# Kernel optimization log

Hardware: AMD Instinct MI355X
Metric: run time of the kernel (lower is better)

## Reference

```python
import jax, jax.numpy as jnp
import numpy as np

N, E, IN = 50000, 800000, 64
HC, FC1, FC2, FC3, OUT = 96, 256, 128, 64, 8
EPS = 1e-5


def setup_inputs() -> dict:
    key = jax.random.key(0)
    ks = jax.random.split(key, 24)
    def lin(k, fi, fo):
        # kaiming_uniform with relu gain: bound = sqrt(6/fi)
        b = np.sqrt(6.0 / fi)
        return jax.random.uniform(k, (fi, fo), jnp.float32, -b, b)
    inp = {
        'x': jax.random.normal(ks[0], (N, IN), jnp.float32),
        'edge_index': jax.random.randint(ks[1], (2, E), 0, N, jnp.int64),
        'w1': lin(ks[2], IN, HC), 'b1': jnp.zeros((HC,), jnp.float32),
        'g1': jax.random.uniform(ks[3], (HC,), jnp.float32, 0.5, 1.5), 'be1': jax.random.normal(ks[4], (HC,), jnp.float32) * 0.1,
        'w2': lin(ks[5], HC, HC), 'b2': jnp.zeros((HC,), jnp.float32),
        'g2': jax.random.uniform(ks[6], (HC,), jnp.float32, 0.5, 1.5), 'be2': jax.random.normal(ks[7], (HC,), jnp.float32) * 0.1,
        'w3': lin(ks[8], HC, HC), 'b3': jnp.zeros((HC,), jnp.float32),
        'g3': jax.random.uniform(ks[9], (HC,), jnp.float32, 0.5, 1.5), 'be3': jax.random.normal(ks[10], (HC,), jnp.float32) * 0.1,
        'lw1': lin(ks[11], HC, FC1), 'lb1': jnp.zeros((FC1,), jnp.float32),
        'lw2': lin(ks[12], FC1, FC2), 'lb2': jnp.zeros((FC2,), jnp.float32),
        'lw3': lin(ks[13], FC2, FC3), 'lb3': jnp.zeros((FC3,), jnp.float32),
        'lw4': lin(ks[14], FC3, OUT), 'lb4': jnp.zeros((OUT,), jnp.float32),
    }
    return inp


def _gcn(x, w, b, src, dst, norm):
    # GCNConv: out[dst] += norm_e * (x @ w)[src]; then + bias
    h = x @ w
    msg = h[src] * norm[:, None]
    return jax.ops.segment_sum(msg, dst, num_segments=N) + b


def _bn_eval(x, g, be):
    # eval-mode BatchNorm1d with running_mean=0, running_var=1
    return x / jnp.sqrt(1.0 + EPS) * g + be


def reference(x, edge_index, w1, b1, g1, be1, w2, b2, g2, be2, w3, b3, g3, be3,
              lw1, lb1, lw2, lb2, lw3, lb3, lw4, lb4):
    loops = jnp.arange(N, dtype=edge_index.dtype)
    src = jnp.concatenate([edge_index[0], loops])
    dst = jnp.concatenate([edge_index[1], loops])
    deg = jax.ops.segment_sum(jnp.ones_like(src, jnp.float32), dst, num_segments=N)
    dinv = jax.lax.rsqrt(deg)  # deg >= 1 due to self loops
    norm = dinv[src] * dinv[dst]

    h = jax.nn.relu(_bn_eval(_gcn(x, w1, b1, src, dst, norm), g1, be1))
    h = jax.nn.relu(_bn_eval(_gcn(h, w2, b2, src, dst, norm), g2, be2))
    h = jax.nn.relu(_bn_eval(_gcn(h, w3, b3, src, dst, norm), g3, be3))
    h = jax.nn.relu(h @ lw1 + lb1)
    h = jax.nn.relu(h @ lw2 + lb2)
    h = jax.nn.relu(h @ lw3 + lb3)
    return h @ lw4 + lb4
```

## Files before the change

kernel.cpp:

```cpp
#include <hip/hip_runtime.h>


#define GN 50000
#define GE 800000
#define NPART 98
#define PSLOT 9216
#define CHK 2048

typedef __attribute__((ext_vector_type(8))) short bf16x8;
typedef __attribute__((ext_vector_type(4))) float floatx4;

__device__ __forceinline__ float ar1_b2f(unsigned short h) {
    return __uint_as_float(((unsigned)h) << 16);
}
__device__ __forceinline__ unsigned short ar1_f2b(float f) {
    unsigned u = __float_as_uint(f);
    u = u + 0x7FFFu + ((u >> 16) & 1u);
    return (unsigned short)(u >> 16);
}

__device__ __forceinline__ int ar1_det64(const int* ei) {
    int l = (int)threadIdx.x & 63;
    int nz = 0;
#pragma unroll
    for (int k = 0; k < 4; k++)
        nz += (ei[2 * (l + 64 * k) + 1] != 0) ? 1 : 0;
#pragma unroll
    for (int o = 1; o < 64; o <<= 1)
        nz += __shfl_xor(nz, o, 64);
    return (nz < 8) ? 1 : 0;
}
__device__ __forceinline__ int ar1_detf32(const unsigned short* xw) {
    int l = (int)threadIdx.x & 63;
    int c = 0;
#pragma unroll
    for (int k = 0; k < 4; k++) {
        unsigned short w = xw[2 * (l + 64 * k)];
        int ex = (w >> 7) & 0xFF;
        if (w == 0 || (ex >= 90 && ex <= 150)) c++;
    }
#pragma unroll
    for (int o = 1; o < 64; o <<= 1)
        c += __shfl_xor(c, o, 64);
    return (c > 200) ? 0 : 1;
}

struct PackAll {
    const void* src[7];
    unsigned short* dst[7];
    int K[7], M[7], start[8];
};
struct SmallCvt {
    const void* src[4];
    float* dst[4];
    int n[4];
    const void* gb[9];
    float* ss[6];
};

__global__ __launch_bounds__(256)
void Arthur1_16458314678864_kernel(PackAll pa, SmallCvt sc,
                                   const int* __restrict__ ei,
                                   const unsigned short* __restrict__ xw,
                                   int* flagI, int* flagF,
                                   int* __restrict__ gcur,
                                   unsigned int* __restrict__ pairs,
                                   unsigned short* __restrict__ xb) {
    int b = (int)blockIdx.x;
    int tid = (int)threadIdx.x;
    if (b < 391) {
        __shared__ int cnt[NPART], base[NPART], cur[NPART];
        for (int i = tid; i < NPART; i += 256) { cnt[i] = 0; cur[i] = 0; }
        int is64 = ar1_det64(ei);
        __syncthreads();
        int e0 = b * CHK;
        unsigned pk[8]; int q[8];
#pragma unroll
        for (int k = 0; k < 8; k++) {
            int e = e0 + k * 256 + tid;
            q[k] = -1; pk[k] = 0;
            if (e < GE) {
                int s = is64 ? ei[2 * e] : ei[e];
                int d = is64 ? ei[2 * (GE + e)] : ei[GE + e];
                if ((unsigned)s < (unsigned)GN && (unsigned)d < (unsigned)GN) {
                    int qq = d >> 9;
                    q[k] = qq;
                    pk[k] = (unsigned)s | ((unsigned)(d & 511) << 17);
                    atomicAdd(&cnt[qq], 1);
                }
            }
        }
        __syncthreads();
        for (int i = tid; i < NPART; i += 256)
            base[i] = (cnt[i] > 0) ? atomicAdd(&gcur[i], cnt[i]) : 0;
        __syncthreads();
#pragma unroll
        for (int k = 0; k < 8; k++) {
            if (q[k] >= 0) {
                int r = base[q[k]] + atomicAdd(&cur[q[k]], 1);
                if (r < PSLOT) pairs[(size_t)q[k] * PSLOT + r] = pk[k];
            }
        }
    } else if (b < 436) {
        int f = ar1_detf32(xw);
        int frag_g = (b - 391) * 4 + (tid >> 6);
        if (frag_g >= 178) return;
        int w = 0;
        while (w < 6 && frag_g >= pa.start[w + 1]) w++;
        int frag = frag_g - pa.start[w];
        int K = pa.K[w], M = pa.M[w];
        int lane = tid & 63;
        int nch = K >> 5;
        int t = frag / nch, c = frag - t * nch;
        int n = t * 16 + (lane & 15);
        int k0 = c * 32 + (lane >> 4) * 8;
        unsigned short* o = pa.dst[w] + ((size_t)frag * 64 + lane) * 8;
        for (int j = 0; j < 8; j++) {
            unsigned short v = 0;
            if (n < M) {
                int idx = (k0 + j) * M + n;
                v = f ? ar1_f2b(((const float*)pa.src[w])[idx])
                      : ((const unsigned short*)pa.src[w])[idx];
            }
            o[j] = v;
        }
    } else if (b == 436) {
        int f = ar1_detf32(xw);
        int i64 = ar1_det64(ei);
        if (tid == 0) { flagI[0] = i64; flagF[0] = f; }
        const float C = 0.9999950000374997f;
        for (int s = 0; s < 4; s++) {
            for (int i = tid; i < sc.n[s]; i += 256) {
                float v = f ? ((const float*)sc.src[s])[i]
                            : ar1_b2f(((const unsigned short*)sc.src[s])[i]);
                sc.dst[s][i] = v;
            }
        }
        for (int k = 0; k < 3; k++) {
            for (int i = tid; i < 96; i += 256) {
                float bb, g, be;
                if (f) {
                    bb = ((const float*)sc.gb[3 * k + 0])[i];
                    g  = ((const float*)sc.gb[3 * k + 1])[i];
                    be = ((const float*)sc.gb[3 * k + 2])[i];
                } else {
                    bb = ar1_b2f(((const unsigned short*)sc.gb[3 * k + 0])[i]);
                    g  = ar1_b2f(((const unsigned short*)sc.gb[3 * k + 1])[i]);
                    be = ar1_b2f(((const unsigned short*)sc.gb[3 * k + 2])[i]);
                }
                sc.ss[2 * k + 0][i] = C * g;
                sc.ss[2 * k + 1][i] = bb * C * g + be;
            }
        }
    } else {
        int f = ar1_detf32(xw);
        size_t t = (size_t)(b - 437) * 256 + (size_t)tid;
        size_t i0 = t * 8;
        if (i0 < (size_t)GN * 64) {
            bf16x8 o;
            if (f) {
                const float* xf = (const float*)xw;
                floatx4 a = *((const floatx4*)(xf + i0));
                floatx4 c = *((const floatx4*)(xf + i0 + 4));
#pragma unroll
                for (int j = 0; j < 4; j++) {
                    o[j]     = (short)ar1_f2b(a[j]);
                    o[4 + j] = (short)ar1_f2b(c[j]);
                }
            } else {
                o = *((const bf16x8*)(xw + i0));
            }
            *((bf16x8*)(xb + i0)) = o;
        }
    }
}

__global__ __launch_bounds__(256)
void ar1_csr(const unsigned int* __restrict__ pairs, const int* __restrict__ gcur,
             int* __restrict__ csr, int* __restrict__ indeg,
             int* __restrict__ offs, float* __restrict__ dinv) {
    __shared__ int ncnt[512], pre[512], cur[512], psum[16], red[256];
    int p = (int)blockIdx.x, tid = (int)threadIdx.x;
    red[tid] = (tid < p && tid < NPART) ? gcur[tid] : 0;
    __syncthreads();
    for (int o = 128; o > 0; o >>= 1) {
        if (tid < o) red[tid] += red[tid + o];
        __syncthreads();
    }
    int gbase = red[0];
    int cntE = gcur[p];
    if (cntE > PSLOT) cntE = PSLOT;
    for (int i = tid; i < 512; i += 256) ncnt[i] = 0;
    __syncthreads();
    const unsigned int* pp = pairs + (size_t)p * PSLOT;
    for (int i = tid; i < cntE; i += 256) atomicAdd(&ncnt[pp[i] >> 17], 1);
    __syncthreads();
    if (tid < 16) {
        int s = 0;
        for (int j = tid * 32; j < tid * 32 + 32; j++) { pre[j] = s; s += ncnt[j]; }
        psum[tid] = s;
    }
    __syncthreads();
    if (tid == 0) {
        int s = 0;
        for (int j = 0; j < 16; j++) { int t = psum[j]; psum[j] = s; s += t; }
    }
    __syncthreads();
    if (tid < 16)
        for (int j = tid * 32; j < tid * 32 + 32; j++) pre[j] += psum[tid];
    __syncthreads();
    for (int j = tid; j < 512; j += 256) {
        cur[j] = pre[j];
        int node = p * 512 + j;
        if (node < GN) {
            indeg[node] = ncnt[j];
            offs[node] = gbase + pre[j];
            dinv[node] = rsqrtf((float)(ncnt[j] + 1));
        }
    }
    __syncthreads();
    for (int i = tid; i < cntE; i += 256) {
        unsigned v = pp[i];
        int r = atomicAdd(&cur[v >> 17], 1);
        csr[gbase + r] = (int)(v & 0x1FFFFu);
    }
}

__global__ __launch_bounds__(1024, 8)
void ar1_ag64g(const unsigned short* __restrict__ Xb, const int* __restrict__ offs,
               const int* __restrict__ indeg, const int* __restrict__ csr,
               const float* __restrict__ dinv,
               const unsigned short* __restrict__ Bp,
               const float* __restrict__ scale, const float* __restrict__ shift,
               unsigned short* __restrict__ C) {
    __shared__ unsigned short AL[16 * 72];
    int tid = (int)threadIdx.x, wv = tid >> 6, lane = tid & 63;
    int nb = (int)blockIdx.x * 16;
    int node = nb + wv;
    int chunk = lane & 7, eslot = lane >> 3;
    float di = dinv[node];
    int off = offs[node], cnt = indeg[node];

    float acc[8];
#pragma unroll
    for (int j = 0; j < 8; j++) acc[j] = 0.f;

    for (int base = 0; base < cnt; base += 16) {
        int ss[2]; float ww[2];
#pragma unroll
        for (int k = 0; k < 2; k++) {
            int e = base + k * 8 + eslot;
            int s = node; float w = 0.f;
            if (e < cnt) {
                s = csr[off + e];
                if ((unsigned)s >= (unsigned)GN) s = node;
                w = dinv[s] * di;
            }
            ss[k] = s; ww[k] = w;
        }
#pragma unroll
        for (int k = 0; k < 2; k++) {
            bf16x8 h = *((const bf16x8*)(Xb + (size_t)ss[k] * 64 + chunk * 8));
#pragma unroll
            for (int j = 0; j < 8; j++)
                acc[j] += ww[k] * ar1_b2f((unsigned short)h[j]);
        }
    }
#pragma unroll
    for (int j = 0; j < 8; j++) {
        acc[j] += __shfl_xor(acc[j], 8, 64);
        acc[j] += __shfl_xor(acc[j], 16, 64);
        acc[j] += __shfl_xor(acc[j], 32, 64);
    }
    if (eslot == 0) {
        bf16x8 h = *((const bf16x8*)(Xb + (size_t)node * 64 + chunk * 8));
        bf16x8 o;
#pragma unroll
        for (int j = 0; j < 8; j++)
            o[j] = (short)ar1_f2b(acc[j] + di * di * ar1_b2f((unsigned short)h[j]));
        *((bf16x8*)(AL + (size_t)wv * 72 + chunk * 8)) = o;
    }
    __syncthreads();

    if (wv < 6) {
        int m = lane & 15, quad = lane >> 4, t = wv;
        floatx4 g = (floatx4){0.f, 0.f, 0.f, 0.f};
#pragma unroll
        for (int c = 0; c < 2; c++) {
            bf16x8 a = *((const bf16x8*)(AL + (size_t)m * 72 + c * 32 + quad * 8));
            bf16x8 bfr = *((const bf16x8*)(Bp + ((size_t)(t * 2 + c) * 64 + lane) * 8));
            g = __builtin_amdgcn_mfma_f32_16x16x32_bf16(a, bfr, g, 0, 0, 0);
        }
#pragma unroll
        for (int r = 0; r < 4; r++) {
            int row = nb + quad * 4 + r;
            int col = t * 16 + m;
            float v = g[r] * scale[col] + shift[col];
            C[(size_t)row * 96 + col] = ar1_f2b(fmaxf(v, 0.f));
        }
    }
}

__global__ __launch_bounds__(1024, 8)
void ar1_ag96g(const unsigned short* __restrict__ H, const int* __restrict__ offs,
               const int* __restrict__ indeg, const int* __restrict__ csr,
               const float* __restrict__ dinv,
               const unsigned short* __restrict__ Bp,
               const float* __restrict__ scale, const float* __restrict__ shift,
               unsigned short* __restrict__ C) {
    __shared__ unsigned short AL[16 * 104];
    int tid = (int)threadIdx.x, wv = tid >> 6, lane = tid & 63;
    int nb = (int)blockIdx.x * 16;
    int node = nb + wv;
    int chunk = lane % 12, eslot = lane / 12;
    int active = (lane < 48) ? 1 : 0;
    float di = dinv[node];
    int off = offs[node], cnt = indeg[node];

    float acc[8];
#pragma unroll
    for (int j = 0; j < 8; j++) acc[j] = 0.f;

    if (active) {
        for (int base = 0; base < cnt; base += 16) {
            int ss[4]; float ww[4]; bf16x8 hh[4];
#pragma unroll
            for (int k = 0; k < 4; k++) {
                int e = base + k * 4 + eslot;
                int s = node; float w = 0.f;
                if (e < cnt) {
                    s = csr[off + e];
                    if ((unsigned)s >= (unsigned)GN) s = node;
                    w = dinv[s] * di;
                }
                ss[k] = s; ww[k] = w;
            }
#pragma unroll
            for (int k = 0; k < 4; k++)
                hh[k] = *((const bf16x8*)(H + (size_t)ss[k] * 96 + chunk * 8));
#pragma unroll
            for (int k = 0; k < 4; k++)
#pragma unroll
                for (int j = 0; j < 8; j++)
                    acc[j] += ww[k] * ar1_b2f((unsigned short)hh[k][j]);
        }
    }
#pragma unroll
    for (int j = 0; j < 8; j++) {
        float a1 = __shfl(acc[j], lane + 12, 64);
        float a2 = __shfl(acc[j], lane + 24, 64);
        float a3 = __shfl(acc[j], lane + 36, 64);
        acc[j] += a1 + a2 + a3;
    }
    if (lane < 12) {
        bf16x8 hs = *((const bf16x8*)(H + (size_t)node * 96 + chunk * 8));
        bf16x8 o;
#pragma unroll
        for (int j = 0; j < 8; j++)
            o[j] = (short)ar1_f2b(acc[j] + di * di * ar1_b2f((unsigned short)hs[j]));
        *((bf16x8*)(AL + (size_t)wv * 104 + chunk * 8)) = o;
    }
    __syncthreads();

    if (wv < 6) {
        int m = lane & 15, quad = lane >> 4, t = wv;
        floatx4 g = (floatx4){0.f, 0.f, 0.f, 0.f};
#pragma unroll
        for (int c = 0; c < 3; c++) {
            bf16x8 a = *((const bf16x8*)(AL + (size_t)m * 104 + c * 32 + quad * 8));
            bf16x8 bfr = *((const bf16x8*)(Bp + ((size_t)(t * 3 + c) * 64 + lane) * 8));
            g = __builtin_amdgcn_mfma_f32_16x16x32_bf16(a, bfr, g, 0, 0, 0);
        }
#pragma unroll
        for (int r = 0; r < 4; r++) {
            int row = nb + quad * 4 + r;
            int col = t * 16 + m;
            float v = g[r] * scale[col] + shift[col];
            C[(size_t)row * 96 + col] = ar1_f2b(fmaxf(v, 0.f));
        }
    }
}

__global__ __launch_bounds__(1024, 8)
void ar1_agmlp(const unsigned short* __restrict__ H, const int* __restrict__ offs,
               const int* __restrict__ indeg, const int* __restrict__ csr,
               const float* __restrict__ dinv,
               const unsigned short* __restrict__ b2w,
               const float* __restrict__ sc3, const float* __restrict__ sh3,
               const unsigned short* __restrict__ b3,
               const unsigned short* __restrict__ b4,
               const unsigned short* __restrict__ b5,
               const unsigned short* __restrict__ b6,
               const float* __restrict__ lb0, const float* __restrict__ lb1,
               const float* __restrict__ lb2, const float* __restrict__ lb3,
               void* __restrict__ out, const int* __restrict__ f32out) {
    __shared__ unsigned short AL[16 * 104];
    __shared__ unsigned short H0[16 * 104];
    __shared__ unsigned short H1[16 * 264];
    __shared__ unsigned short H2[16 * 136];
    __shared__ unsigned short H3[16 * 72];
    int tid = (int)threadIdx.x, wv = tid >> 6, lane = tid & 63;
    int nb = (int)blockIdx.x * 16;
    int node = nb + wv;
    int m = lane & 15, quad = lane >> 4;

    {
        int chunk = lane % 12, eslot = lane / 12;
        int active = (lane < 48) ? 1 : 0;
        float di = dinv[node];
        int off = offs[node], cnt = indeg[node];
        float acc[8];
#pragma unroll
        for (int j = 0; j < 8; j++) acc[j] = 0.f;
        if (active) {
            for (int base = 0; base < cnt; base += 16) {
                int ss[4]; float ww[4]; bf16x8 hh[4];
#pragma unroll
                for (int k = 0; k < 4; k++) {
                    int e = base + k * 4 + eslot;
                    int s = node; float w = 0.f;
                    if (e < cnt) {
                        s = csr[off + e];
                        if ((unsigned)s >= (unsigned)GN) s = node;
                        w = dinv[s] * di;
                    }
                    ss[k] = s; ww[k] = w;
                }
#pragma unroll
                for (int k = 0; k < 4; k++)
                    hh[k] = *((const bf16x8*)(H + (size_t)ss[k] * 96 + chunk * 8));
#pragma unroll
                for (int k = 0; k < 4; k++)
#pragma unroll
                    for (int j = 0; j < 8; j++)
                        acc[j] += ww[k] * ar1_b2f((unsigned short)hh[k][j]);
            }
        }
#pragma unroll
        for (int j = 0; j < 8; j++) {
            float a1 = __shfl(acc[j], lane + 12, 64);
            float a2 = __shfl(acc[j], lane + 24, 64);
            float a3 = __shfl(acc[j], lane + 36, 64);
            acc[j] += a1 + a2 + a3;
        }
        if (lane < 12) {
            bf16x8 hs = *((const bf16x8*)(H + (size_t)node * 96 + chunk * 8));
            bf16x8 o;
#pragma unroll
            for (int j = 0; j < 8; j++)
                o[j] = (short)ar1_f2b(acc[j] + di * di * ar1_b2f((unsigned short)hs[j]));
            *((bf16x8*)(AL + (size_t)wv * 104 + chunk * 8)) = o;
        }
    }
    __syncthreads();

    if (wv < 6) {
        int t = wv;
        floatx4 g = (floatx4){0.f, 0.f, 0.f, 0.f};
#pragma unroll
        for (int c = 0; c < 3; c++) {
            bf16x8 a = *((const bf16x8*)(AL + (size_t)m * 104 + c * 32 + quad * 8));
            bf16x8 bfr = *((const bf16x8*)(b2w + ((size_t)(t * 3 + c) * 64 + lane) * 8));
            g = __builtin_amdgcn_mfma_f32_16x16x32_bf16(a, bfr, g, 0, 0, 0);
        }
#pragma unroll
        for (int r = 0; r < 4; r++) {
            int col = t * 16 + m;
            float v = g[r] * sc3[col] + sh3[col];
            H0[(quad * 4 + r) * 104 + col] = ar1_f2b(fmaxf(v, 0.f));
        }
    }
    __syncthreads();

    {
        int t = wv;
        floatx4 g = (floatx4){0.f, 0.f, 0.f, 0.f};
#pragma unroll
        for (int c = 0; c < 3; c++) {
            bf16x8 a = *((const bf16x8*)(H0 + (size_t)m * 104 + c * 32 + quad * 8));
            bf16x8 bfr = *((const bf16x8*)(b3 + ((size_t)(t * 3 + c) * 64 + lane) * 8));
            g = __builtin_amdgcn_mfma_f32_16x16x32_bf16(a, bfr, g, 0, 0, 0);
        }
#pragma unroll
        for (int r = 0; r < 4; r++) {
            int col = t * 16 + m;
            H1[(quad * 4 + r) * 264 + col] = ar1_f2b(fmaxf(g[r] + lb0[col], 0.f));
        }
    }
    __syncthreads();

    if (wv < 8) {
        int t = wv;
        floatx4 g = (floatx4){0.f, 0.f, 0.f, 0.f};
#pragma unroll
        for (int c = 0; c < 8; c++) {
            bf16x8 a = *((const bf16x8*)(H1 + (size_t)m * 264 + c * 32 + quad * 8));
            bf16x8 bfr = *((const bf16x8*)(b4 + ((size_t)(t * 8 + c) * 64 + lane) * 8));
            g = __builtin_amdgcn_mfma_f32_16x16x32_bf16(a, bfr, g, 0, 0, 0);
        }
#pragma unroll
        for (int r = 0; r < 4; r++) {
            int col = t * 16 + m;
            H2[(quad * 4 + r) * 136 + col] = ar1_f2b(fmaxf(g[r] + lb1[col], 0.f));
        }
    }
    __syncthreads();

    if (wv < 4) {
        int t = wv;
        floatx4 g = (floatx4){0.f, 0.f, 0.f, 0.f};
#pragma unroll
        for (int c = 0; c < 4; c++) {
            bf16x8 a = *((const bf16x8*)(H2 + (size_t)m * 136 + c * 32 + quad * 8));
            bf16x8 bfr = *((const bf16x8*)(b5 + ((size_t)(t * 4 + c) * 64 + lane) * 8));
            g = __builtin_amdgcn_mfma_f32_16x16x32_bf16(a, bfr, g, 0, 0, 0);
        }
#pragma unroll
        for (int r = 0; r < 4; r++) {
            int col = t * 16 + m;
            H3[(quad * 4 + r) * 72 + col] = ar1_f2b(fmaxf(g[r] + lb2[col], 0.f));
        }
    }
    __syncthreads();

    if (wv == 0) {
        floatx4 g = (floatx4){0.f, 0.f, 0.f, 0.f};
#pragma unroll
        for (int c = 0; c < 2; c++) {
            bf16x8 a = *((const bf16x8*)(H3 + (size_t)m * 72 + c * 32 + quad * 8));
            bf16x8 bfr = *((const bf16x8*)(b6 + ((size_t)c * 64 + lane) * 8));
            g = __builtin_amdgcn_mfma_f32_16x16x32_bf16(a, bfr, g, 0, 0, 0);
        }
        int wf32 = f32out[0];
#pragma unroll
        for (int r = 0; r < 4; r++) {
            int row = nb + quad * 4 + r;
            if (m < 8) {
                float v = g[r] + lb3[m];
                if (wf32) ((float*)out)[(size_t)row * 8 + m] = v;
                else ((unsigned short*)out)[(size_t)row * 8 + m] = ar1_f2b(v);
            }
        }
    }
}

extern "C" void kernel_launch(void* const* d_in, const int* in_sizes, int n_in,
                              void* d_out, int out_size, void* d_ws, size_t ws_size,
                              hipStream_t stream) {
    (void)in_sizes; (void)n_in; (void)out_size;

    char* p = (char*)d_ws;
    unsigned short* bufA = (unsigned short*)p; p += (size_t)GN * 96 * 2;
    unsigned short* bufB = (unsigned short*)p; p += (size_t)GN * 96 * 2;
    unsigned short* xb   = (unsigned short*)p; p += (size_t)GN * 64 * 2;
    unsigned int* pairs = (unsigned int*)p; p += (size_t)NPART * PSLOT * 4;
    int* indeg  = (int*)p;    p += (size_t)GN * 4;
    int* offs   = (int*)p;    p += (size_t)GN * 4;
    float* dinv = (float*)p;  p += (size_t)GN * 4;
    int* csr    = (int*)p;    p += (size_t)GE * 4;
    int* gcur   = (int*)p;    p += 1024;
    int* flagI  = (int*)p;    p += 1024;
    int* flagF  = (int*)p;    p += 1024;
    unsigned short* bpArena = (unsigned short*)p; p += 91136 * 2;
    float* fArena = (float*)p; p += 2048 * 4;
    size_t need = (size_t)(p - (char*)d_ws);
    if (ws_size < need) {
        hipMemsetAsync(d_out, 0x41, (size_t)GN * 8 * 2, stream);
        return;
    }

    unsigned short* bp[7];
    int bpn[7] = {6144, 9216, 9216, 24576, 32768, 8192, 1024};
    {
        unsigned short* q = bpArena;
        for (int i = 0; i < 7; i++) { bp[i] = q; q += bpn[i]; }
    }

    float* lb[4]; float* ss[6];
    {
        float* q = fArena;
        int ln[4] = {256, 128, 64, 8};
        for (int i = 0; i < 4; i++) { lb[i] = q; q += ln[i]; }
        for (int i = 0; i < 6; i++) { ss[i] = q; q += 96; }
    }

    const int* ei = (const int*)d_in[1];
    const unsigned short* xw = (const unsigned short*)d_in[0];

    hipMemsetAsync(gcur, 0, NPART * 4, stream);
    {
        PackAll pa;
        int wsrc[7] = {2, 6, 10, 14, 16, 18, 20};
        int Ks[7] = {64, 96, 96, 96, 256, 128, 64};
        int Ms[7] = {96, 96, 96, 256, 128, 64, 8};
        int cum = 0;
        for (int i = 0; i < 7; i++) {
            pa.src[i] = d_in[wsrc[i]]; pa.dst[i] = bp[i];
            pa.K[i] = Ks[i]; pa.M[i] = Ms[i];
            pa.start[i] = cum;
            cum += (Ms[i] + 15) / 16 * (Ks[i] / 32);
        }
        pa.start[7] = cum;
        SmallCvt sc;
        int lsrc[4] = {15, 17, 19, 21};
        int ln[4] = {256, 128, 64, 8};
        for (int i = 0; i < 4; i++) { sc.src[i] = d_in[lsrc[i]]; sc.dst[i] = lb[i]; sc.n[i] = ln[i]; }
        int gsrc[9] = {3, 4, 5, 7, 8, 9, 11, 12, 13};
        for (int i = 0; i < 9; i++) sc.gb[i] = d_in[gsrc[i]];
        for (int i = 0; i < 6; i++) sc.ss[i] = ss[i];
        Arthur1_16458314678864_kernel<<<2000, 256, 0, stream>>>(
            pa, sc, ei, xw, flagI, flagF, gcur, pairs, xb);
    }
    ar1_csr<<<NPART, 256, 0, stream>>>(pairs, gcur, csr, indeg, offs, dinv);

    const int FB = GN / 16;

    ar1_ag64g<<<FB, 1024, 0, stream>>>(xb, offs, indeg, csr, dinv,
                                       bp[0], ss[0], ss[1], bufA);
    ar1_ag96g<<<FB, 1024, 0, stream>>>(bufA, offs, indeg, csr, dinv,
                                       bp[1], ss[2], ss[3], bufB);
    ar1_agmlp<<<FB, 1024, 0, stream>>>(bufB, offs, indeg, csr, dinv,
                                       bp[2], ss[4], ss[5],
                                       bp[3], bp[4], bp[5], bp[6],
                                       lb[0], lb[1], lb[2], lb[3], d_out, flagF);
}
```

Before: 281.2 us.

## Prescale stored features by dinv and pad with a zero sentinel row

The producing kernels now multiply their outputs by dinv[row], so the next layer's aggregation sums neighbour features unweighted and applies dinv of the destination once at the end. This removes the per-edge dinv gather and multiply in the 96-wide layers. Out-of-range edge slots now point to a zeroed sentinel row at index GN instead of taking a masked branch, which lets the gather loops double their unroll and issue more loads at once. The cost is extra workspace for the padding rows and one more multiply per stored output.

```diff
diff --git a/kernel.cpp b/kernel.cpp
--- a/kernel.cpp
+++ b/kernel.cpp
@@ -65,7 +65,10 @@
                                    int* flagI, int* flagF,
                                    int* __restrict__ gcur,
                                    unsigned int* __restrict__ pairs,
-                                   unsigned short* __restrict__ xb) {
+                                   unsigned short* __restrict__ xb,
+                                   unsigned short* __restrict__ bufA,
+                                   unsigned short* __restrict__ bufB,
+                                   float* __restrict__ dinvp) {
     int b = (int)blockIdx.x;
     int tid = (int)threadIdx.x;
     if (b < 391) {
@@ -127,7 +130,12 @@
     } else if (b == 436) {
         int f = ar1_detf32(xw);
         int i64 = ar1_det64(ei);
-        if (tid == 0) { flagI[0] = i64; flagF[0] = f; }
+        if (tid == 0) { flagI[0] = i64; flagF[0] = f; dinvp[GN] = 0.f; }
+        if (tid < 96) {
+            bufA[(size_t)GN * 96 + tid] = 0;
+            bufB[(size_t)GN * 96 + tid] = 0;
+        }
+        if (tid >= 96 && tid < 160) xb[(size_t)GN * 64 + (tid - 96)] = 0;
         const float C = 0.9999950000374997f;
         for (int s = 0; s < 4; s++) {
             for (int i = tid; i < sc.n[s]; i += 256) {
@@ -245,26 +253,24 @@
 #pragma unroll
     for (int j = 0; j < 8; j++) acc[j] = 0.f;
 
-    for (int base = 0; base < cnt; base += 16) {
-        int ss[2]; float ww[2];
-#pragma unroll
-        for (int k = 0; k < 2; k++) {
+    for (int base = 0; base < cnt; base += 32) {
+        int ss[4]; float ww[4];
+#pragma unroll
+        for (int k = 0; k < 4; k++) {
             int e = base + k * 8 + eslot;
-            int s = node; float w = 0.f;
-            if (e < cnt) {
-                s = csr[off + e];
-                if ((unsigned)s >= (unsigned)GN) s = node;
-                w = dinv[s] * di;
-            }
-            ss[k] = s; ww[k] = w;
-        }
-#pragma unroll
-        for (int k = 0; k < 2; k++) {
-            bf16x8 h = *((const bf16x8*)(Xb + (size_t)ss[k] * 64 + chunk * 8));
+            int s = (e < cnt) ? csr[off + e] : GN;
+            ss[k] = s;
+            ww[k] = dinv[s] * di;
+        }
+        bf16x8 hh[4];
+#pragma unroll
+        for (int k = 0; k < 4; k++)
+            hh[k] = *((const bf16x8*)(Xb + (size_t)ss[k] * 64 + chunk * 8));
+#pragma unroll
+        for (int k = 0; k < 4; k++)
 #pragma unroll
             for (int j = 0; j < 8; j++)
-                acc[j] += ww[k] * ar1_b2f((unsigned short)h[j]);
-        }
+                acc[j] += ww[k] * ar1_b2f((unsigned short)hh[k][j]);
     }
 #pragma unroll
     for (int j = 0; j < 8; j++) {
@@ -296,7 +302,7 @@
             int row = nb + quad * 4 + r;
             int col = t * 16 + m;
             float v = g[r] * scale[col] + shift[col];
-            C[(size_t)row * 96 + col] = ar1_f2b(fmaxf(v, 0.f));
+            C[(size_t)row * 96 + col] = ar1_f2b(dinv[row] * fmaxf(v, 0.f));
         }
     }
 }
@@ -313,7 +319,6 @@
     int nb = (int)blockIdx.x * 16;
     int node = nb + wv;
     int chunk = lane % 12, eslot = lane / 12;
-    int active = (lane < 48) ? 1 : 0;
     float di = dinv[node];
     int off = offs[node], cnt = indeg[node];
 
@@ -321,28 +326,23 @@
 #pragma unroll
     for (int j = 0; j < 8; j++) acc[j] = 0.f;
 
-    if (active) {
-        for (int base = 0; base < cnt; base += 16) {
-            int ss[4]; float ww[4]; bf16x8 hh[4];
-#pragma unroll
-            for (int k = 0; k < 4; k++) {
+    if (lane < 48) {
+        for (int base = 0; base < cnt; base += 32) {
+            int ss[8];
+#pragma unroll
+            for (int k = 0; k < 8; k++) {
                 int e = base + k * 4 + eslot;
-                int s = node; float w = 0.f;
-                if (e < cnt) {
-                    s = csr[off + e];
-                    if ((unsigned)s >= (unsigned)GN) s = node;
-                    w = dinv[s] * di;
-                }
-                ss[k] = s; ww[k] = w;
-            }
-#pragma unroll
-            for (int k = 0; k < 4; k++)
+                ss[k] = (e < cnt) ? csr[off + e] : GN;
+            }
+            bf16x8 hh[8];
+#pragma unroll
+            for (int k = 0; k < 8; k++)
                 hh[k] = *((const bf16x8*)(H + (size_t)ss[k] * 96 + chunk * 8));
 #pragma unroll
-            for (int k = 0; k < 4; k++)
+            for (int k = 0; k < 8; k++)
 #pragma unroll
                 for (int j = 0; j < 8; j++)
-                    acc[j] += ww[k] * ar1_b2f((unsigned short)hh[k][j]);
+                    acc[j] += ar1_b2f((unsigned short)hh[k][j]);
         }
     }
 #pragma unroll
@@ -357,7 +357,7 @@
         bf16x8 o;
 #pragma unroll
         for (int j = 0; j < 8; j++)
-            o[j] = (short)ar1_f2b(acc[j] + di * di * ar1_b2f((unsigned short)hs[j]));
+            o[j] = (short)ar1_f2b(di * (acc[j] + ar1_b2f((unsigned short)hs[j])));
         *((bf16x8*)(AL + (size_t)wv * 104 + chunk * 8)) = o;
     }
     __syncthreads();
@@ -376,7 +376,7 @@
             int row = nb + quad * 4 + r;
             int col = t * 16 + m;
             float v = g[r] * scale[col] + shift[col];
-            C[(size_t)row * 96 + col] = ar1_f2b(fmaxf(v, 0.f));
+            C[(size_t)row * 96 + col] = ar1_f2b(dinv[row] * fmaxf(v, 0.f));
         }
     }
 }
@@ -406,34 +406,28 @@
 
     {
         int chunk = lane % 12, eslot = lane / 12;
-        int active = (lane < 48) ? 1 : 0;
         float di = dinv[node];
         int off = offs[node], cnt = indeg[node];
         float acc[8];
 #pragma unroll
         for (int j = 0; j < 8; j++) acc[j] = 0.f;
-        if (active) {
-            for (int base = 0; base < cnt; base += 16) {
-                int ss[4]; float ww[4]; bf16x8 hh[4];
-#pragma unroll
-                for (int k = 0; k < 4; k++) {
+        if (lane < 48) {
+            for (int base = 0; base < cnt; base += 32) {
+                int ss[8];
+#pragma unroll
+                for (int k = 0; k < 8; k++) {
                     int e = base + k * 4 + eslot;
-                    int s = node; float w = 0.f;
-                    if (e < cnt) {
-                        s = csr[off + e];
-                        if ((unsigned)s >= (unsigned)GN) s = node;
-                        w = dinv[s] * di;
-                    }
-                    ss[k] = s; ww[k] = w;
+                    ss[k] = (e < cnt) ? csr[off + e] : GN;
                 }
-#pragma unroll
-                for (int k = 0; k < 4; k++)
+                bf16x8 hh[8];
+#pragma unroll
+                for (int k = 0; k < 8; k++)
                     hh[k] = *((const bf16x8*)(H + (size_t)ss[k] * 96 + chunk * 8));
 #pragma unroll
-                for (int k = 0; k < 4; k++)
+                for (int k = 0; k < 8; k++)
 #pragma unroll
                     for (int j = 0; j < 8; j++)
-                        acc[j] += ww[k] * ar1_b2f((unsigned short)hh[k][j]);
+                        acc[j] += ar1_b2f((unsigned short)hh[k][j]);
             }
         }
 #pragma unroll
@@ -448,7 +442,7 @@
             bf16x8 o;
 #pragma unroll
             for (int j = 0; j < 8; j++)
-                o[j] = (short)ar1_f2b(acc[j] + di * di * ar1_b2f((unsigned short)hs[j]));
+                o[j] = (short)ar1_f2b(di * (acc[j] + ar1_b2f((unsigned short)hs[j])));
             *((bf16x8*)(AL + (size_t)wv * 104 + chunk * 8)) = o;
         }
     }
@@ -550,13 +544,13 @@
     (void)in_sizes; (void)n_in; (void)out_size;
 
     char* p = (char*)d_ws;
-    unsigned short* bufA = (unsigned short*)p; p += (size_t)GN * 96 * 2;
-    unsigned short* bufB = (unsigned short*)p; p += (size_t)GN * 96 * 2;
-    unsigned short* xb   = (unsigned short*)p; p += (size_t)GN * 64 * 2;
+    unsigned short* bufA = (unsigned short*)p; p += (size_t)(GN + 1) * 96 * 2;
+    unsigned short* bufB = (unsigned short*)p; p += (size_t)(GN + 1) * 96 * 2;
+    unsigned short* xb   = (unsigned short*)p; p += (size_t)(GN + 1) * 64 * 2;
     unsigned int* pairs = (unsigned int*)p; p += (size_t)NPART * PSLOT * 4;
     int* indeg  = (int*)p;    p += (size_t)GN * 4;
     int* offs   = (int*)p;    p += (size_t)GN * 4;
-    float* dinv = (float*)p;  p += (size_t)GN * 4;
+    float* dinv = (float*)p;  p += (size_t)GN * 4 + 64;
     int* csr    = (int*)p;    p += (size_t)GE * 4;
     int* gcur   = (int*)p;    p += 1024;
     int* flagI  = (int*)p;    p += 1024;
@@ -609,7 +603,7 @@
         for (int i = 0; i < 9; i++) sc.gb[i] = d_in[gsrc[i]];
         for (int i = 0; i < 6; i++) sc.ss[i] = ss[i];
         Arthur1_16458314678864_kernel<<<2000, 256, 0, stream>>>(
-            pa, sc, ei, xw, flagI, flagF, gcur, pairs, xb);
+            pa, sc, ei, xw, flagI, flagF, gcur, pairs, xb, bufA, bufB, dinv);
     }
     ar1_csr<<<NPART, 256, 0, stream>>>(pairs, gcur, csr, indeg, offs, dinv);
 
```

Result: no change. 281.9 us (+0.3%).
